# Optimization experiments

Hardware: AMD Instinct MI355X
Metric: run time of the kernel (lower is better)

The kernel has to match this reference:

```python
import jax, jax.numpy as jnp
import numpy as np


def _lstm_step(h, c, x, kernel, rec_kernel, bias):
    # Keras LSTMCell: gate order i, f, g(candidate), o
    z = x @ kernel + h @ rec_kernel + bias  # [B, 4u]
    i, f, g, o = jnp.split(z, 4, axis=-1)
    i = jax.nn.sigmoid(i)
    f = jax.nn.sigmoid(f)
    g = jnp.tanh(g)
    o = jax.nn.sigmoid(o)
    c2 = f * c + i * g
    h2 = o * jnp.tanh(c2)
    return h2, c2


def setup_inputs() -> dict:
    key = jax.random.key(0)
    ks = jax.random.split(key, 4)
    B, S, F, U = 2048, 64, 3, 512
    OUT_NOTES = 64
    inputs = jax.random.normal(ks[0], (B, S, F), dtype=jnp.float32)
    kernel = jax.random.normal(ks[1], (F, 4 * U), dtype=jnp.float32) * 0.1
    rec_kernel = jax.random.normal(ks[2], (U, 4 * U), dtype=jnp.float32) * 0.05
    bias = jnp.zeros((4 * U,), dtype=jnp.float32)
    dense_w = jax.random.normal(ks[3], (U, F), dtype=jnp.float32) * 0.1
    dense_b = jnp.zeros((F,), dtype=jnp.float32)
    return {"inputs": inputs, "kernel": kernel, "rec_kernel": rec_kernel,
            "bias": bias, "dense_w": dense_w, "dense_b": dense_b}


def reference(inputs, kernel, rec_kernel, bias, dense_w, dense_b):
    OUT_NOTES = 64
    B = inputs.shape[0]
    U = rec_kernel.shape[0]
    h0 = jnp.zeros((B, U), dtype=inputs.dtype)
    c0 = jnp.zeros((B, U), dtype=inputs.dtype)

    # warmup: run LSTM over the input sequence, keep final state
    def warm_step(carry, x_t):
        h, c = carry
        h2, c2 = _lstm_step(h, c, x_t, kernel, rec_kernel, bias)
        return (h2, c2), None

    xs = jnp.swapaxes(inputs, 0, 1)  # [S, B, F]
    (h, c), _ = jax.lax.scan(warm_step, (h0, c0), xs)
    pred0 = h @ dense_w + dense_b  # [B, 3]

    def ar_step(carry, _):
        pred, h, c = carry
        h2, c2 = _lstm_step(h, c, pred, kernel, rec_kernel, bias)
        pred2 = h2 @ dense_w + dense_b
        return (pred2, h2, c2), pred2

    _, preds = jax.lax.scan(ar_step, (pred0, h, c), None, length=OUT_NOTES - 1)
    # tf.stack(predictions) stacks along axis 0 -> [out_notes, B, 3]
    return jnp.concatenate([pred0[None], preds], axis=0)
```

## Files before the change

### kernel.cpp

```cpp
#include <hip/hip_runtime.h>
#include <hip/hip_fp16.h>

typedef _Float16 f16;
typedef __attribute__((ext_vector_type(8))) _Float16 f16x8;
typedef __attribute__((ext_vector_type(16))) float f32x16;

#define NB 2048
#define SEQ 64
#define NF 3
#define NU 512
#define N4U 2048
#define NSTEP 127
#define WT_LD 520

#define SM_WT_BYTES (128 * WT_LD * 2)
#define SM_XS_OFF   SM_WT_BYTES
#define SM_TOTAL    (SM_XS_OFF + 128 * 3 * 4)

#define WS_PP_OFF   (16 * 1024)
#define WS_H_OFF    (1u << 20)
#define PP_PAR_STRIDE (16 * 16 * 128 * 3)
#define PP_BT_STRIDE  (16 * 128 * 3)
#define PP_UG_STRIDE  (128 * 3)

__device__ __forceinline__ float fast_rcp(float x) { return __builtin_amdgcn_rcpf(x); }
__device__ __forceinline__ float sigf(float x) { return fast_rcp(1.f + __expf(-x)); }
__device__ __forceinline__ float tanhf_fast(float x) {
    float a = fabsf(x);
    float e = __expf(-2.f * a);
    float t = (1.f - e) * fast_rcp(1.f + e);
    return copysignf(t, x);
}

__global__ __launch_bounds__(256, 1)
void lstm_feedback_kernel(const float* __restrict__ inputs, const float* __restrict__ kernw,
                          const float* __restrict__ rec, const float* __restrict__ bias,
                          const float* __restrict__ dw, const float* __restrict__ db,
                          float* __restrict__ out, float* __restrict__ pp,
                          f16* __restrict__ hbuf, unsigned* __restrict__ bar)
{
    extern __shared__ char smem[];
    f16* Wt = (f16*)smem;
    float* x_s = (float*)(smem + SM_XS_OFF);

    const int tid = threadIdx.x;
    const int bid = blockIdx.x;
    const int xcd = bid & 7;
    const int jj  = bid >> 3;
    const int bt  = (xcd << 1) | (jj & 1);
    const int ug  = jj >> 1;
    const int uBase = ug * 32;
    const int bBase = bt * 128;
    const int w  = tid >> 6;
    const int l  = tid & 63;
    const int l31 = l & 31;
    const int hf  = l >> 5;
    unsigned* mybar = bar + bt * 256;

    {
        const int c  = tid & 127;
        const int kk = tid >> 7;
        const int gcol = ((c >> 5) * 512) + uBase + (c & 31);
        for (int k = kk; k < NU; k += 2)
            Wt[c * WT_LD + k] = (f16)rec[k * N4U + gcol];
    }

    float kr[4][3], br[4], dwr[3], dbr[3];
    #pragma unroll
    for (int ct = 0; ct < 4; ++ct) {
        const int gcol = ct * 512 + uBase + l31;
        #pragma unroll
        for (int f = 0; f < 3; ++f) kr[ct][f] = kernw[f * N4U + gcol];
        br[ct] = bias[gcol];
    }
    {
        const int u = uBase + l31;
        #pragma unroll
        for (int j = 0; j < 3; ++j) { dwr[j] = dw[u * 3 + j]; dbr[j] = db[j]; }
    }
    __syncthreads();

    float c_reg[16];
    #pragma unroll
    for (int r = 0; r < 16; ++r) c_reg[r] = 0.f;

    const size_t HB = (size_t)NB * NU;
    const int bW = bBase + w * 32;
    const size_t aoff = (size_t)(bW + l31) * NU + hf * 8;
    const f16* bptr = Wt + (size_t)l31 * WT_LD + hf * 8;

    for (int s = 0; s < NSTEP; ++s) {
        if (s > 0) {
            if (tid == 0) {
                const unsigned tgt = (unsigned)s * 16u;
                while (__hip_atomic_load(mybar, __ATOMIC_RELAXED, __HIP_MEMORY_SCOPE_AGENT) < tgt) {}
                __threadfence();
            }
            __syncthreads();
        }

        if (tid < 128) {
            float v0, v1, v2;
            if (s < SEQ) {
                const float* xp = inputs + ((size_t)(bBase + tid) * SEQ + s) * NF;
                v0 = xp[0]; v1 = xp[1]; v2 = xp[2];
            } else {
                const float* p = pp + (size_t)((s + 1) & 1) * PP_PAR_STRIDE
                               + bt * PP_BT_STRIDE + tid * 3;
                v0 = dbr[0]; v1 = dbr[1]; v2 = dbr[2];
                #pragma unroll
                for (int g = 0; g < 16; ++g) {
                    v0 += p[g * PP_UG_STRIDE + 0];
                    v1 += p[g * PP_UG_STRIDE + 1];
                    v2 += p[g * PP_UG_STRIDE + 2];
                }
                if (ug == 0) {
                    float* o = out + ((size_t)(s - SEQ) * NB + bBase + tid) * 3;
                    o[0] = v0; o[1] = v1; o[2] = v2;
                }
            }
            x_s[tid * 3 + 0] = v0;
            x_s[tid * 3 + 1] = v1;
            x_s[tid * 3 + 2] = v2;
        }
        __syncthreads();

        f32x16 acc0 = {}, acc1 = {}, acc2 = {}, acc3 = {};
        if (s > 0) {
            const f16* ap = hbuf + (size_t)(s & 1) * HB + aoff;
            #pragma unroll 8
            for (int kt = 0; kt < 32; ++kt) {
                const int k0 = kt * 16;
                f16x8 a  = *(const f16x8*)(ap + k0);
                f16x8 b0 = *(const f16x8*)(bptr + 0 * 32 * WT_LD + k0);
                f16x8 b1 = *(const f16x8*)(bptr + 1 * 32 * WT_LD + k0);
                f16x8 b2 = *(const f16x8*)(bptr + 2 * 32 * WT_LD + k0);
                f16x8 b3 = *(const f16x8*)(bptr + 3 * 32 * WT_LD + k0);
                acc0 = __builtin_amdgcn_mfma_f32_32x32x16_f16(a, b0, acc0, 0, 0, 0);
                acc1 = __builtin_amdgcn_mfma_f32_32x32x16_f16(a, b1, acc1, 0, 0, 0);
                acc2 = __builtin_amdgcn_mfma_f32_32x32x16_f16(a, b2, acc2, 0, 0, 0);
                acc3 = __builtin_amdgcn_mfma_f32_32x32x16_f16(a, b3, acc3, 0, 0, 0);
            }
        }

        f16* hw = hbuf + (size_t)((s & 1) ^ 1) * HB;
        const int n_out = s - (SEQ - 1);
        float* ppw = pp + (size_t)(s & 1) * PP_PAR_STRIDE + bt * PP_BT_STRIDE + ug * PP_UG_STRIDE;
        #pragma unroll
        for (int r = 0; r < 16; ++r) {
            const int mrow = (r & 3) + ((r >> 2) << 3) + (hf << 2);
            const int mloc = (w << 5) + mrow;
            const float x0 = x_s[mloc * 3 + 0];
            const float x1 = x_s[mloc * 3 + 1];
            const float x2 = x_s[mloc * 3 + 2];
            float z0 = acc0[r] + x0 * kr[0][0] + x1 * kr[0][1] + x2 * kr[0][2] + br[0];
            float z1 = acc1[r] + x0 * kr[1][0] + x1 * kr[1][1] + x2 * kr[1][2] + br[1];
            float z2 = acc2[r] + x0 * kr[2][0] + x1 * kr[2][1] + x2 * kr[2][2] + br[2];
            float z3 = acc3[r] + x0 * kr[3][0] + x1 * kr[3][1] + x2 * kr[3][2] + br[3];
            const float gi = sigf(z0);
            const float gf = sigf(z1);
            const float gg = tanhf_fast(z2);
            const float go = sigf(z3);
            const float cv = gf * c_reg[r] + gi * gg;
            c_reg[r] = cv;
            const float h2 = go * tanhf_fast(cv);
            hw[(size_t)(bBase + mloc) * NU + uBase + l31] = (f16)h2;

            if (n_out >= 0) {
                #pragma unroll
                for (int j = 0; j < 3; ++j) {
                    float v = h2 * dwr[j];
                    #pragma unroll
                    for (int m = 1; m < 32; m <<= 1) v += __shfl_xor(v, m, 64);
                    if (l31 == r) ppw[mloc * 3 + j] = v;
                }
            }
        }

        __syncthreads();
        if (tid == 0) {
            __threadfence();
            __hip_atomic_fetch_add(mybar, 1u, __ATOMIC_RELAXED, __HIP_MEMORY_SCOPE_AGENT);
        }
    }

    if (ug == 0) {
        if (tid == 0) {
            while (__hip_atomic_load(mybar, __ATOMIC_RELAXED, __HIP_MEMORY_SCOPE_AGENT)
                   < (unsigned)NSTEP * 16u) {}
            __threadfence();
        }
        __syncthreads();
        if (tid < 128) {
            const float* p = pp + bt * PP_BT_STRIDE + tid * 3;
            float v0 = dbr[0], v1 = dbr[1], v2 = dbr[2];
            #pragma unroll
            for (int g = 0; g < 16; ++g) {
                v0 += p[g * PP_UG_STRIDE + 0];
                v1 += p[g * PP_UG_STRIDE + 1];
                v2 += p[g * PP_UG_STRIDE + 2];
            }
            float* o = out + ((size_t)63 * NB + bBase + tid) * 3;
            o[0] = v0; o[1] = v1; o[2] = v2;
        }
    }
}

extern "C" void kernel_launch(void* const* d_in, const int* in_sizes, int n_in,
                              void* d_out, int out_size, void* d_ws, size_t ws_size,
                              hipStream_t stream) {
    const float* inputs = (const float*)d_in[0];
    const float* kernw  = (const float*)d_in[1];
    const float* rec    = (const float*)d_in[2];
    const float* bias   = (const float*)d_in[3];
    const float* dw     = (const float*)d_in[4];
    const float* db     = (const float*)d_in[5];
    float* out = (float*)d_out;

    unsigned* bar = (unsigned*)d_ws;
    float* pp  = (float*)((char*)d_ws + WS_PP_OFF);
    f16* hbuf  = (f16*)((char*)d_ws + WS_H_OFF);

    hipMemsetAsync(d_ws, 0, 16 * 1024, stream);

    hipFuncSetAttribute(reinterpret_cast<const void*>(lstm_feedback_kernel),
                        hipFuncAttributeMaxDynamicSharedMemorySize, SM_TOTAL);

    void* args[] = { (void*)&inputs, (void*)&kernw, (void*)&rec, (void*)&bias,
                     (void*)&dw, (void*)&db, (void*)&out, (void*)&pp,
                     (void*)&hbuf, (void*)&bar };
    hipLaunchCooperativeKernel(reinterpret_cast<const void*>(lstm_feedback_kernel),
                               dim3(256), dim3(256), args, SM_TOTAL, stream);
}
```

Before: 2.908 ms.

## Replace atomic counter barrier with per-block flags and L2-coherent stores

Swaps the per-batch-tile atomic fetch_add counter barrier for per-block step flags. Sixteen threads poll the 16 producer flags in parallel, so arrival no longer serializes through atomics on one counter. The full __threadfence is replaced by sc1 stores for h, atomic stores for partial predictions, an s_waitcnt before publishing the flag, and a buffer_inv on the reader side. This is meant to cut the per-step inter-block synchronization latency, at the risk of subtle memory-ordering bugs if the cache-scope choices are wrong.

```diff
diff --git a/kernel.cpp b/kernel.cpp
--- a/kernel.cpp
+++ b/kernel.cpp
@@ -37,7 +37,7 @@
                           const float* __restrict__ rec, const float* __restrict__ bias,
                           const float* __restrict__ dw, const float* __restrict__ db,
                           float* __restrict__ out, float* __restrict__ pp,
-                          f16* __restrict__ hbuf, unsigned* __restrict__ bar)
+                          f16* __restrict__ hbuf, unsigned* __restrict__ flags)
 {
     extern __shared__ char smem[];
     f16* Wt = (f16*)smem;
@@ -55,7 +55,7 @@
     const int l  = tid & 63;
     const int l31 = l & 31;
     const int hf  = l >> 5;
-    unsigned* mybar = bar + bt * 256;
+    unsigned* myflags = flags + bt * 32;
 
     {
         const int c  = tid & 127;
@@ -91,11 +91,15 @@
 
     for (int s = 0; s < NSTEP; ++s) {
         if (s > 0) {
-            if (tid == 0) {
-                const unsigned tgt = (unsigned)s * 16u;
-                while (__hip_atomic_load(mybar, __ATOMIC_RELAXED, __HIP_MEMORY_SCOPE_AGENT) < tgt) {}
-                __threadfence();
-            }
+            if (tid < 16) {
+                const unsigned* fp = myflags + tid;
+                unsigned v;
+                do {
+                    v = __hip_atomic_load(fp, __ATOMIC_RELAXED, __HIP_MEMORY_SCOPE_AGENT);
+                } while (v < (unsigned)s);
+            }
+            __syncthreads();
+            if (w == 0) asm volatile("buffer_inv sc1" ::: "memory");
             __syncthreads();
         }
 
@@ -164,7 +168,12 @@
             const float cv = gf * c_reg[r] + gi * gg;
             c_reg[r] = cv;
             const float h2 = go * tanhf_fast(cv);
-            hw[(size_t)(bBase + mloc) * NU + uBase + l31] = (f16)h2;
+            {
+                f16* ha = hw + (size_t)(bBase + mloc) * NU + uBase + l31;
+                unsigned hb = (unsigned)__builtin_bit_cast(unsigned short, (f16)h2);
+                asm volatile("global_store_short %0, %1, off sc1"
+                             :: "v"(ha), "v"(hb) : "memory");
+            }
 
             if (n_out >= 0) {
                 #pragma unroll
@@ -172,24 +181,30 @@
                     float v = h2 * dwr[j];
                     #pragma unroll
                     for (int m = 1; m < 32; m <<= 1) v += __shfl_xor(v, m, 64);
-                    if (l31 == r) ppw[mloc * 3 + j] = v;
+                    if (l31 == r)
+                        __hip_atomic_store(&ppw[mloc * 3 + j], v,
+                                           __ATOMIC_RELAXED, __HIP_MEMORY_SCOPE_AGENT);
                 }
             }
         }
 
-        __syncthreads();
-        if (tid == 0) {
-            __threadfence();
-            __hip_atomic_fetch_add(mybar, 1u, __ATOMIC_RELAXED, __HIP_MEMORY_SCOPE_AGENT);
-        }
+        asm volatile("s_waitcnt vmcnt(0)" ::: "memory");
+        __syncthreads();
+        if (tid == 0)
+            __hip_atomic_store(myflags + ug, (unsigned)(s + 1),
+                               __ATOMIC_RELAXED, __HIP_MEMORY_SCOPE_AGENT);
     }
 
     if (ug == 0) {
-        if (tid == 0) {
-            while (__hip_atomic_load(mybar, __ATOMIC_RELAXED, __HIP_MEMORY_SCOPE_AGENT)
-                   < (unsigned)NSTEP * 16u) {}
-            __threadfence();
-        }
+        if (tid < 16) {
+            const unsigned* fp = myflags + tid;
+            unsigned v;
+            do {
+                v = __hip_atomic_load(fp, __ATOMIC_RELAXED, __HIP_MEMORY_SCOPE_AGENT);
+            } while (v < (unsigned)NSTEP);
+        }
+        __syncthreads();
+        if (w == 0) asm volatile("buffer_inv sc1" ::: "memory");
         __syncthreads();
         if (tid < 128) {
             const float* p = pp + bt * PP_BT_STRIDE + tid * 3;
@@ -217,7 +232,7 @@
     const float* db     = (const float*)d_in[5];
     float* out = (float*)d_out;
 
-    unsigned* bar = (unsigned*)d_ws;
+    unsigned* flags = (unsigned*)d_ws;
     float* pp  = (float*)((char*)d_ws + WS_PP_OFF);
     f16* hbuf  = (f16*)((char*)d_ws + WS_H_OFF);
 
@@ -228,7 +243,7 @@
 
     void* args[] = { (void*)&inputs, (void*)&kernw, (void*)&rec, (void*)&bias,
                      (void*)&dw, (void*)&db, (void*)&out, (void*)&pp,
-                     (void*)&hbuf, (void*)&bar };
+                     (void*)&hbuf, (void*)&flags };
     hipLaunchCooperativeKernel(reinterpret_cast<const void*>(lstm_feedback_kernel),
                                dim3(256), dim3(256), args, SM_TOTAL, stream);
 }
```

After: 2.560 ms. -12.0%, faster.
